# Kernel optimization log

Measured on AMD Instinct MI355X. Metric: run time of the kernel, lower is better.

## Reference

```python
import jax, jax.numpy as jnp
import numpy as np

N_NODES = 100000


def _gcn_layer(x, W, b, row, col, norm, n_nodes):
    # x: [N, Fin], W: [Fin, Fout]. GCN: A_hat @ (x W) + b with symmetric norm.
    xw = x @ W                                   # [N, Fout]
    msg = xw[row] * norm[:, None]                # [E+N, Fout] gathered messages
    agg = jax.ops.segment_sum(msg, col, num_segments=n_nodes)  # scatter-add at dst
    return agg + b


def setup_inputs() -> dict:
    key = jax.random.key(0)
    ks = jax.random.split(key, 5)
    N, E = N_NODES, 1600000
    Fin, F1, F2, C = 512, 64, 128, 40
    x = jax.random.normal(ks[0], (N, Fin), dtype=jnp.float32)
    edge_index = jax.random.randint(ks[1], (2, E), 0, N, dtype=jnp.int64)
    W1 = jax.random.normal(ks[2], (Fin, F1), dtype=jnp.float32) / np.sqrt(Fin)
    W2 = jax.random.normal(ks[3], (F1, F2), dtype=jnp.float32) / np.sqrt(F1)
    W3 = jax.random.normal(ks[4], (F2, C), dtype=jnp.float32) / np.sqrt(F2)
    return {
        "x": x, "edge_index": edge_index,
        "W1": W1, "b1": jnp.zeros((F1,), jnp.float32),
        "W2": W2, "b2": jnp.zeros((F2,), jnp.float32),
        "W3": W3, "b3": jnp.zeros((C,), jnp.float32),
    }


def reference(x, edge_index, W1, b1, W2, b2, W3, b3):
    N = x.shape[0]
    # Add self-loops (GCNConv default add_self_loops=True)
    loop = jnp.arange(N, dtype=edge_index.dtype)
    row = jnp.concatenate([edge_index[0], loop])  # source nodes
    col = jnp.concatenate([edge_index[1], loop])  # destination nodes
    # Symmetric degree normalization: deg computed at destination with self-loops
    deg = jax.ops.segment_sum(jnp.ones_like(col, dtype=x.dtype), col, num_segments=N)
    dis = jax.lax.rsqrt(deg)                      # deg >= 1 due to self-loops
    norm = dis[row] * dis[col]                    # [E+N]

    h1 = jax.nn.relu(_gcn_layer(x, W1, b1, row, col, norm, N))
    # dropout is identity (training=False)
    h2 = jax.nn.relu(_gcn_layer(h1, W2, b2, row, col, norm, N))
    h3 = _gcn_layer(h2, W3, b3, row, col, norm, N)
    return jax.nn.log_softmax(h3, axis=1)
```

## Files before the change

kernel.cpp:

```cpp
#include <hip/hip_runtime.h>
#include <math.h>


typedef __attribute__((ext_vector_type(8))) short short8;
typedef __attribute__((ext_vector_type(4))) float f32x4;

__device__ __forceinline__ unsigned short f2bf(float f) {
    unsigned int u = __float_as_uint(f);
    unsigned int r = (u + 0x7fffu + ((u >> 16) & 1u)) >> 16;
    return (unsigned short)r;
}
__device__ __forceinline__ float bflo(unsigned int u) { return __uint_as_float(u << 16); }
__device__ __forceinline__ float bfhi(unsigned int u) { return __uint_as_float(u & 0xffff0000u); }


__global__ void zero2_kernel(int* a, int* b, int n) {
    int i = blockIdx.x * 256 + threadIdx.x;
    if (i < n) { a[i] = 0; b[i] = 0; }
}

__global__ void count_kernel(const int* __restrict__ col, int* __restrict__ cnt, int E) {
    int e = blockIdx.x * 256 + threadIdx.x;
    if (e < E) atomicAdd(&cnt[col[e]], 1);
}

__global__ void scan1_kernel(const int* __restrict__ cnt, int* __restrict__ out,
                             int* __restrict__ bsums, int n) {
    __shared__ int s[1024];
    int i = blockIdx.x * 1024 + threadIdx.x;
    int v = (i < n) ? cnt[i] : 0;
    s[threadIdx.x] = v;
    __syncthreads();
    for (int off = 1; off < 1024; off <<= 1) {
        int t = 0;
        if ((int)threadIdx.x >= off) t = s[threadIdx.x - off];
        __syncthreads();
        if ((int)threadIdx.x >= off) s[threadIdx.x] += t;
        __syncthreads();
    }
    if (i < n) out[i] = s[threadIdx.x] - v;
    if (threadIdx.x == 1023) bsums[blockIdx.x] = s[1023];
}

__global__ void scan2_kernel(int* bsums, int nb) {
    __shared__ int s[128];
    int v = ((int)threadIdx.x < nb) ? bsums[threadIdx.x] : 0;
    s[threadIdx.x] = v;
    __syncthreads();
    for (int off = 1; off < 128; off <<= 1) {
        int t = 0;
        if ((int)threadIdx.x >= off) t = s[threadIdx.x - off];
        __syncthreads();
        if ((int)threadIdx.x >= off) s[threadIdx.x] += t;
        __syncthreads();
    }
    if ((int)threadIdx.x < nb) bsums[threadIdx.x] = s[threadIdx.x] - v;
}

__global__ void scan3d_kernel(int* __restrict__ ptr, const int* __restrict__ bsums,
                              const int* __restrict__ cnt, float* __restrict__ dis,
                              int n, int E) {
    int i = blockIdx.x * 1024 + threadIdx.x;
    if (i < n) {
        ptr[i] += bsums[blockIdx.x];
        dis[i] = rsqrtf((float)(cnt[i] + 1));
    }
    if (i == 0) ptr[n] = E;
}

__global__ void fill_kernel(const int* __restrict__ row, const int* __restrict__ col,
                            const int* __restrict__ ptr, int* __restrict__ fillc,
                            const float* __restrict__ dis, uint2* __restrict__ csr_en, int E) {
    int e = blockIdx.x * 256 + threadIdx.x;
    if (e < E) {
        int c = col[e];
        int r = row[e];
        int p = ptr[c] + atomicAdd(&fillc[c], 1);
        uint2 en;
        en.x = (unsigned int)r;
        en.y = __float_as_uint(dis[r] * dis[c]);
        csr_en[p] = en;
    }
}

__device__ __forceinline__ void wprep_one(const float* W, unsigned short* out,
                                          int KS, int FOUT, int t) {
    int i = t & 7;
    int l = (t >> 3) & 63;
    int g = t >> 9;
    int ks = g % KS;
    int nt = g / KS;
    int k = ks * 32 + (l >> 4) * 8 + i;
    int c = nt * 16 + (l & 15);
    out[t] = (c < FOUT) ? f2bf(W[(size_t)k * FOUT + c]) : (unsigned short)0;
}

__global__ void wprep_all_kernel(const float* __restrict__ W1, const float* __restrict__ W2,
                                 const float* __restrict__ W3,
                                 unsigned short* __restrict__ Wf1, unsigned short* __restrict__ Wf2,
                                 unsigned short* __restrict__ Wf3) {
    int t = blockIdx.x * 256 + threadIdx.x;
    if (t < 32768)       wprep_one(W1, Wf1, 16, 64, t);
    else if (t < 40960)  wprep_one(W2, Wf2, 2, 128, t - 32768);
    else if (t < 47104)  wprep_one(W3, Wf3, 4, 40, t - 40960);
}

template <int K, int FOUT, int NT>
__global__ __launch_bounds__(256) void gemm1_kernel(const float* __restrict__ Ap,
                                                    const unsigned short* __restrict__ Wf,
                                                    unsigned short* __restrict__ Y, int N) {
    constexpr int KS = K / 32;
    const int lane = threadIdx.x & 63;
    const int wid = threadIdx.x >> 6;
    const int rbase = blockIdx.x * 64 + wid * 16;
    const int rA = rbase + (lane & 15);
    const bool va = rA < N;
    const int khalf = lane >> 4;

    f32x4 acc[NT];
#pragma unroll
    for (int nt = 0; nt < NT; nt++)
#pragma unroll
        for (int j = 0; j < 4; j++) acc[nt][j] = 0.f;

    for (int ks = 0; ks < KS; ks++) {
        short8 afr;
        const float4* Arow = (const float4*)(Ap + (size_t)rA * K + ks * 32 + khalf * 8);
        float4 x0, x1;
        if (va) { x0 = Arow[0]; x1 = Arow[1]; }
        else    { x0 = make_float4(0, 0, 0, 0); x1 = x0; }
        afr[0] = (short)f2bf(x0.x); afr[1] = (short)f2bf(x0.y);
        afr[2] = (short)f2bf(x0.z); afr[3] = (short)f2bf(x0.w);
        afr[4] = (short)f2bf(x1.x); afr[5] = (short)f2bf(x1.y);
        afr[6] = (short)f2bf(x1.z); afr[7] = (short)f2bf(x1.w);
#pragma unroll
        for (int nt = 0; nt < NT; nt++) {
            short8 bfr = *(const short8*)(Wf + (((size_t)nt * KS + ks) * 64 + lane) * 8);
            acc[nt] = __builtin_amdgcn_mfma_f32_16x16x32_bf16(afr, bfr, acc[nt], 0, 0, 0);
        }
    }

    const int rD0 = rbase + (lane >> 4) * 4;
    const int colb = lane & 15;
#pragma unroll
    for (int nt = 0; nt < NT; nt++) {
        int col = nt * 16 + colb;
#pragma unroll
        for (int i = 0; i < 4; i++) {
            int rD = rD0 + i;
            if (rD < N) Y[(size_t)rD * FOUT + col] = f2bf(acc[nt][i]);
        }
    }
}

__global__ __launch_bounds__(256) void gemm23_kernel(const unsigned short* __restrict__ A,
                                                     const unsigned short* __restrict__ Wf2,
                                                     const float* __restrict__ b2,
                                                     const unsigned short* __restrict__ Wf3,
                                                     unsigned short* __restrict__ Y, int N) {
    __shared__ unsigned short hs[4][16][136];
    const int lane = threadIdx.x & 63;
    const int wid = threadIdx.x >> 6;
    const int rbase = blockIdx.x * 64 + wid * 16;
    const int rA = rbase + (lane & 15);
    const bool va = rA < N;
    const int khalf = lane >> 4;

    f32x4 acc2[8];
#pragma unroll
    for (int nt = 0; nt < 8; nt++)
#pragma unroll
        for (int j = 0; j < 4; j++) acc2[nt][j] = 0.f;

#pragma unroll
    for (int ks = 0; ks < 2; ks++) {
        short8 afr;
        if (va) afr = *(const short8*)(A + (size_t)rA * 64 + ks * 32 + khalf * 8);
        else {
#pragma unroll
            for (int j = 0; j < 8; j++) afr[j] = 0;
        }
#pragma unroll
        for (int nt = 0; nt < 8; nt++) {
            short8 bfr = *(const short8*)(Wf2 + (((size_t)nt * 2 + ks) * 64 + lane) * 8);
            acc2[nt] = __builtin_amdgcn_mfma_f32_16x16x32_bf16(afr, bfr, acc2[nt], 0, 0, 0);
        }
    }

    const int rD = (lane >> 4) * 4;
    const int colb = lane & 15;
#pragma unroll
    for (int nt = 0; nt < 8; nt++) {
        int c = nt * 16 + colb;
        float bv = b2[c];
#pragma unroll
        for (int j = 0; j < 4; j++)
            hs[wid][rD + j][c] = f2bf(fmaxf(acc2[nt][j] + bv, 0.f));
    }
    __syncthreads();

    f32x4 acc3[3];
#pragma unroll
    for (int nt = 0; nt < 3; nt++)
#pragma unroll
        for (int j = 0; j < 4; j++) acc3[nt][j] = 0.f;

    const int r = lane & 15;
#pragma unroll
    for (int ks = 0; ks < 4; ks++) {
        short8 afr = *(const short8*)&hs[wid][r][ks * 32 + khalf * 8];
#pragma unroll
        for (int nt = 0; nt < 3; nt++) {
            short8 bfr = *(const short8*)(Wf3 + (((size_t)nt * 4 + ks) * 64 + lane) * 8);
            acc3[nt] = __builtin_amdgcn_mfma_f32_16x16x32_bf16(afr, bfr, acc3[nt], 0, 0, 0);
        }
    }

#pragma unroll
    for (int nt = 0; nt < 3; nt++) {
        int col = nt * 16 + colb;
        if (col < 40) {
#pragma unroll
            for (int i = 0; i < 4; i++) {
                int rr = rbase + rD + i;
                if (rr < N) Y[(size_t)rr * 40 + col] = f2bf(acc3[nt][i]);
            }
        }
    }
}

template <bool BR>
__global__ __launch_bounds__(256) void agg64_kernel(const unsigned int* __restrict__ XW,
                                                    const float* __restrict__ bias,
                                                    const int* __restrict__ ptr,
                                                    const uint2* __restrict__ EN,
                                                    unsigned int* __restrict__ Y, int N) {
    const int lane = threadIdx.x & 63;
    const int wid = threadIdx.x >> 6;
    const int n = blockIdx.x * 4 + wid;
    if (n >= N) return;
    const int s = lane >> 3;
    const int q = lane & 7;

    const int e0 = ptr[n], e1 = ptr[n + 1];
    const float selfw = 1.0f / (float)(e1 - e0 + 1);

    float acc[8];
    if (s == 0) {
        const uint4 u = *(const uint4*)(XW + (size_t)n * 32 + q * 4);
        acc[0] = selfw * bflo(u.x); acc[1] = selfw * bfhi(u.x);
        acc[2] = selfw * bflo(u.y); acc[3] = selfw * bfhi(u.y);
        acc[4] = selfw * bflo(u.z); acc[5] = selfw * bfhi(u.z);
        acc[6] = selfw * bflo(u.w); acc[7] = selfw * bfhi(u.w);
    } else {
#pragma unroll
        for (int j = 0; j < 8; j++) acc[j] = 0.f;
    }

    for (int eb = e0; eb < e1; eb += 64) {
        int cnt = e1 - eb; if (cnt > 64) cnt = 64;
        uint2 en;
        if (lane < cnt) en = EN[eb + lane];
        else { en.x = 0; en.y = 0; }
#pragma unroll 2
        for (int k = s; k < cnt; k += 8) {
            int r = __shfl((int)en.x, k);
            float nrm = __uint_as_float((unsigned int)__shfl((int)en.y, k));
            const uint4 u = *(const uint4*)(XW + (size_t)r * 32 + q * 4);
            acc[0] += nrm * bflo(u.x); acc[1] += nrm * bfhi(u.x);
            acc[2] += nrm * bflo(u.y); acc[3] += nrm * bfhi(u.y);
            acc[4] += nrm * bflo(u.z); acc[5] += nrm * bfhi(u.z);
            acc[6] += nrm * bflo(u.w); acc[7] += nrm * bfhi(u.w);
        }
    }

#pragma unroll
    for (int off = 8; off < 64; off <<= 1)
#pragma unroll
        for (int j = 0; j < 8; j++) acc[j] += __shfl_xor(acc[j], off);

    if (lane < 8) {
        float v[8];
        if (BR) {
            const float4 b0 = *((const float4*)bias + lane * 2);
            const float4 b1 = *((const float4*)bias + lane * 2 + 1);
            v[0] = fmaxf(acc[0] + b0.x, 0.f); v[1] = fmaxf(acc[1] + b0.y, 0.f);
            v[2] = fmaxf(acc[2] + b0.z, 0.f); v[3] = fmaxf(acc[3] + b0.w, 0.f);
            v[4] = fmaxf(acc[4] + b1.x, 0.f); v[5] = fmaxf(acc[5] + b1.y, 0.f);
            v[6] = fmaxf(acc[6] + b1.z, 0.f); v[7] = fmaxf(acc[7] + b1.w, 0.f);
        } else {
#pragma unroll
            for (int j = 0; j < 8; j++) v[j] = acc[j];
        }
        uint4 o;
        o.x = (unsigned int)f2bf(v[0]) | ((unsigned int)f2bf(v[1]) << 16);
        o.y = (unsigned int)f2bf(v[2]) | ((unsigned int)f2bf(v[3]) << 16);
        o.z = (unsigned int)f2bf(v[4]) | ((unsigned int)f2bf(v[5]) << 16);
        o.w = (unsigned int)f2bf(v[6]) | ((unsigned int)f2bf(v[7]) << 16);
        *(uint4*)(Y + (size_t)n * 32 + lane * 4) = o;
    }
}

__global__ __launch_bounds__(256) void agg40lsm_kernel(const unsigned int* __restrict__ XW,
                                                       const float* __restrict__ bias,
                                                       const int* __restrict__ ptr,
                                                       const uint2* __restrict__ EN,
                                                       float* __restrict__ out, int N) {
    const int lane = threadIdx.x & 63;
    const int wid = threadIdx.x >> 6;
    const int n = blockIdx.x * 4 + wid;
    if (n >= N) return;
    const int s = lane >> 4;
    const int c = lane & 15;
    const bool act = (c < 10);

    const int e0 = ptr[n], e1 = ptr[n + 1];
    const float selfw = 1.0f / (float)(e1 - e0 + 1);

    float acc[4] = {0.f, 0.f, 0.f, 0.f};
    if (s == 0 && act) {
        const uint2 u = *(const uint2*)(XW + (size_t)n * 20 + c * 2);
        acc[0] = selfw * bflo(u.x); acc[1] = selfw * bfhi(u.x);
        acc[2] = selfw * bflo(u.y); acc[3] = selfw * bfhi(u.y);
    }

    for (int eb = e0; eb < e1; eb += 64) {
        int cnt = e1 - eb; if (cnt > 64) cnt = 64;
        uint2 en;
        if (lane < cnt) en = EN[eb + lane];
        else { en.x = 0; en.y = 0; }
#pragma unroll 2
        for (int k = s; k < cnt; k += 4) {
            int r = __shfl((int)en.x, k);
            float nrm = __uint_as_float((unsigned int)__shfl((int)en.y, k));
            if (act) {
                const uint2 u = *(const uint2*)(XW + (size_t)r * 20 + c * 2);
                acc[0] += nrm * bflo(u.x); acc[1] += nrm * bfhi(u.x);
                acc[2] += nrm * bflo(u.y); acc[3] += nrm * bfhi(u.y);
            }
        }
    }

#pragma unroll
    for (int off = 16; off < 64; off <<= 1)
#pragma unroll
        for (int j = 0; j < 4; j++) acc[j] += __shfl_xor(acc[j], off);

    float v[4];
    float m = -INFINITY;
    if (lane < 16 && act) {
        const float4 b = *((const float4*)bias + c);
        v[0] = acc[0] + b.x; v[1] = acc[1] + b.y;
        v[2] = acc[2] + b.z; v[3] = acc[3] + b.w;
        m = fmaxf(fmaxf(v[0], v[1]), fmaxf(v[2], v[3]));
    }
#pragma unroll
    for (int off = 32; off; off >>= 1) m = fmaxf(m, __shfl_xor(m, off));
    float ex = 0.f;
    if (lane < 16 && act)
        ex = expf(v[0] - m) + expf(v[1] - m) + expf(v[2] - m) + expf(v[3] - m);
#pragma unroll
    for (int off = 32; off; off >>= 1) ex += __shfl_xor(ex, off);
    float ls = logf(ex);
    if (lane < 16 && act) {
        float4 o;
        o.x = v[0] - m - ls; o.y = v[1] - m - ls;
        o.z = v[2] - m - ls; o.w = v[3] - m - ls;
        *(float4*)(out + (size_t)n * 40 + c * 4) = o;
    }
}


extern "C" void kernel_launch(void* const* d_in, const int* in_sizes, int n_in,
                              void* d_out, int out_size, void* d_ws, size_t ws_size,
                              hipStream_t stream) {
    const float* x  = (const float*)d_in[0];
    const int*   ei = (const int*)d_in[1];
    const float* W1 = (const float*)d_in[2];
    const float* b1 = (const float*)d_in[3];
    const float* W2 = (const float*)d_in[4];
    const float* b2 = (const float*)d_in[5];
    const float* W3 = (const float*)d_in[6];
    const float* b3 = (const float*)d_in[7];
    const int N = in_sizes[0] / 512;
    const int E = in_sizes[1] / 2;
    const int* row = ei;
    const int* col = ei + E;

    char* p = (char*)d_ws;
    auto alloc = [&](size_t bytes) {
        void* r = (void*)p;
        p += (bytes + 255) & ~(size_t)255;
        return r;
    };
    float* dis    = (float*)alloc((size_t)N * 4);
    int*   cnt    = (int*)alloc((size_t)N * 4);
    int*   ptr    = (int*)alloc((size_t)(N + 1) * 4);
    int*   fillc  = (int*)alloc((size_t)N * 4);
    int*   bsums  = (int*)alloc(1024);
    uint2* csr_en = (uint2*)alloc((size_t)E * 8);
    unsigned short* Wf1 = (unsigned short*)alloc(4 * 16 * 64 * 8 * 2);
    unsigned short* Wf2 = (unsigned short*)alloc(8 * 2 * 64 * 8 * 2);
    unsigned short* Wf3 = (unsigned short*)alloc(3 * 4 * 64 * 8 * 2);
    unsigned short* xw1 = (unsigned short*)alloc((size_t)N * 64 * 2);
    unsigned short* h1  = (unsigned short*)alloc((size_t)N * 64 * 2);
    unsigned short* a2  = (unsigned short*)alloc((size_t)N * 64 * 2);
    unsigned short* xw3 = (unsigned short*)alloc((size_t)N * 40 * 2);
    float* out = (float*)d_out;

    zero2_kernel<<<(N + 255) / 256, 256, 0, stream>>>(cnt, fillc, N);
    count_kernel<<<(E + 255) / 256, 256, 0, stream>>>(col, cnt, E);
    int nb = (N + 1023) / 1024;
    scan1_kernel<<<nb, 1024, 0, stream>>>(cnt, ptr, bsums, N);
    scan2_kernel<<<1, 128, 0, stream>>>(bsums, nb);
    scan3d_kernel<<<nb, 1024, 0, stream>>>(ptr, bsums, cnt, dis, N, E);
    fill_kernel<<<(E + 255) / 256, 256, 0, stream>>>(row, col, ptr, fillc, dis, csr_en, E);

    wprep_all_kernel<<<(47104 + 255) / 256, 256, 0, stream>>>(W1, W2, W3, Wf1, Wf2, Wf3);

    const int ggrid = (N + 63) / 64;
    const int ngrid = (N + 3) / 4;

    gemm1_kernel<512, 64, 4><<<ggrid, 256, 0, stream>>>(x, Wf1, xw1, N);
    agg64_kernel<true><<<ngrid, 256, 0, stream>>>((const unsigned int*)xw1, b1, ptr, csr_en,
                                                  (unsigned int*)h1, N);
    agg64_kernel<false><<<ngrid, 256, 0, stream>>>((const unsigned int*)h1, nullptr, ptr, csr_en,
                                                   (unsigned int*)a2, N);
    gemm23_kernel<<<ggrid, 256, 0, stream>>>(a2, Wf2, b2, Wf3, xw3, N);
    agg40lsm_kernel<<<ngrid, 256, 0, stream>>>((const unsigned int*)xw3, b3, ptr, csr_en, out, N);
}
```

Baseline: 379.1 us.

## Fuse degree count into GEMM1 launch and widen per-lane aggregation work

Zeroing of the count buffers moves into the weight-prep kernel. The destination-degree atomic count now runs as extra blocks inside the first GEMM launch, so the count and the GEMM can overlap and two launches go away. Both aggregation kernels change their lane mapping: 4 lanes now cover one row and 16 edges are processed in parallel per wavefront, with more features per lane. This raises memory-level parallelism on the gathers, at the cost of more registers and longer shuffle reductions.

```diff
diff --git a/kernel.cpp b/kernel.cpp
--- a/kernel.cpp
+++ b/kernel.cpp
@@ -13,15 +13,29 @@
 __device__ __forceinline__ float bflo(unsigned int u) { return __uint_as_float(u << 16); }
 __device__ __forceinline__ float bfhi(unsigned int u) { return __uint_as_float(u & 0xffff0000u); }
 
-
-__global__ void zero2_kernel(int* a, int* b, int n) {
-    int i = blockIdx.x * 256 + threadIdx.x;
-    if (i < n) { a[i] = 0; b[i] = 0; }
-}
-
-__global__ void count_kernel(const int* __restrict__ col, int* __restrict__ cnt, int E) {
-    int e = blockIdx.x * 256 + threadIdx.x;
-    if (e < E) atomicAdd(&cnt[col[e]], 1);
+__device__ __forceinline__ void wprep_one(const float* W, unsigned short* out,
+                                          int KS, int FOUT, int t) {
+    int i = t & 7;
+    int l = (t >> 3) & 63;
+    int g = t >> 9;
+    int ks = g % KS;
+    int nt = g / KS;
+    int k = ks * 32 + (l >> 4) * 8 + i;
+    int c = nt * 16 + (l & 15);
+    out[t] = (c < FOUT) ? f2bf(W[(size_t)k * FOUT + c]) : (unsigned short)0;
+}
+
+__global__ void prep_kernel(const float* __restrict__ W1, const float* __restrict__ W2,
+                            const float* __restrict__ W3,
+                            unsigned short* __restrict__ Wf1, unsigned short* __restrict__ Wf2,
+                            unsigned short* __restrict__ Wf3,
+                            int* __restrict__ cnt, int* __restrict__ fillc, int N) {
+    int t = blockIdx.x * 256 + threadIdx.x;
+    if (t < 32768)       wprep_one(W1, Wf1, 16, 64, t);
+    else if (t < 40960)  wprep_one(W2, Wf2, 2, 128, t - 32768);
+    else if (t < 47104)  wprep_one(W3, Wf3, 4, 40, t - 40960);
+    if (t < N) cnt[t] = 0;
+    else if (t < 2 * N) fillc[t - N] = 0;
 }
 
 __global__ void scan1_kernel(const int* __restrict__ cnt, int* __restrict__ out,
@@ -83,36 +97,22 @@
     }
 }
 
-__device__ __forceinline__ void wprep_one(const float* W, unsigned short* out,
-                                          int KS, int FOUT, int t) {
-    int i = t & 7;
-    int l = (t >> 3) & 63;
-    int g = t >> 9;
-    int ks = g % KS;
-    int nt = g / KS;
-    int k = ks * 32 + (l >> 4) * 8 + i;
-    int c = nt * 16 + (l & 15);
-    out[t] = (c < FOUT) ? f2bf(W[(size_t)k * FOUT + c]) : (unsigned short)0;
-}
-
-__global__ void wprep_all_kernel(const float* __restrict__ W1, const float* __restrict__ W2,
-                                 const float* __restrict__ W3,
-                                 unsigned short* __restrict__ Wf1, unsigned short* __restrict__ Wf2,
-                                 unsigned short* __restrict__ Wf3) {
-    int t = blockIdx.x * 256 + threadIdx.x;
-    if (t < 32768)       wprep_one(W1, Wf1, 16, 64, t);
-    else if (t < 40960)  wprep_one(W2, Wf2, 2, 128, t - 32768);
-    else if (t < 47104)  wprep_one(W3, Wf3, 4, 40, t - 40960);
-}
-
-template <int K, int FOUT, int NT>
-__global__ __launch_bounds__(256) void gemm1_kernel(const float* __restrict__ Ap,
-                                                    const unsigned short* __restrict__ Wf,
-                                                    unsigned short* __restrict__ Y, int N) {
-    constexpr int KS = K / 32;
+__global__ __launch_bounds__(256) void gemm1c_kernel(const float* __restrict__ Ap,
+                                                     const unsigned short* __restrict__ Wf,
+                                                     unsigned short* __restrict__ Y, int N,
+                                                     const int* __restrict__ col,
+                                                     int* __restrict__ cnt, int E, int cgrid) {
+    int bid = blockIdx.x;
+    if (bid < cgrid) {
+        int e = bid * 256 + threadIdx.x;
+        if (e < E) atomicAdd(&cnt[col[e]], 1);
+        return;
+    }
+    bid -= cgrid;
+    constexpr int K = 512, FOUT = 64, NT = 4, KS = K / 32;
     const int lane = threadIdx.x & 63;
     const int wid = threadIdx.x >> 6;
-    const int rbase = blockIdx.x * 64 + wid * 16;
+    const int rbase = bid * 64 + wid * 16;
     const int rA = rbase + (lane & 15);
     const bool va = rA < N;
     const int khalf = lane >> 4;
@@ -144,11 +144,11 @@
     const int colb = lane & 15;
 #pragma unroll
     for (int nt = 0; nt < NT; nt++) {
-        int col = nt * 16 + colb;
+        int c = nt * 16 + colb;
 #pragma unroll
         for (int i = 0; i < 4; i++) {
             int rD = rD0 + i;
-            if (rD < N) Y[(size_t)rD * FOUT + col] = f2bf(acc[nt][i]);
+            if (rD < N) Y[(size_t)rD * FOUT + c] = f2bf(acc[nt][i]);
         }
     }
 }
@@ -218,12 +218,12 @@
 
 #pragma unroll
     for (int nt = 0; nt < 3; nt++) {
-        int col = nt * 16 + colb;
-        if (col < 40) {
+        int c = nt * 16 + colb;
+        if (c < 40) {
 #pragma unroll
             for (int i = 0; i < 4; i++) {
                 int rr = rbase + rD + i;
-                if (rr < N) Y[(size_t)rr * 40 + col] = f2bf(acc3[nt][i]);
+                if (rr < N) Y[(size_t)rr * 40 + c] = f2bf(acc3[nt][i]);
             }
         }
     }
@@ -239,22 +239,27 @@
     const int wid = threadIdx.x >> 6;
     const int n = blockIdx.x * 4 + wid;
     if (n >= N) return;
-    const int s = lane >> 3;
-    const int q = lane & 7;
+    const int s = lane >> 2;
+    const int q = lane & 3;
 
     const int e0 = ptr[n], e1 = ptr[n + 1];
     const float selfw = 1.0f / (float)(e1 - e0 + 1);
 
-    float acc[8];
+    float acc[16];
     if (s == 0) {
-        const uint4 u = *(const uint4*)(XW + (size_t)n * 32 + q * 4);
-        acc[0] = selfw * bflo(u.x); acc[1] = selfw * bfhi(u.x);
-        acc[2] = selfw * bflo(u.y); acc[3] = selfw * bfhi(u.y);
-        acc[4] = selfw * bflo(u.z); acc[5] = selfw * bfhi(u.z);
-        acc[6] = selfw * bflo(u.w); acc[7] = selfw * bfhi(u.w);
+        const uint4 u0 = *(const uint4*)(XW + (size_t)n * 32 + q * 4);
+        const uint4 u1 = *(const uint4*)(XW + (size_t)n * 32 + 16 + q * 4);
+        acc[0] = selfw * bflo(u0.x); acc[1] = selfw * bfhi(u0.x);
+        acc[2] = selfw * bflo(u0.y); acc[3] = selfw * bfhi(u0.y);
+        acc[4] = selfw * bflo(u0.z); acc[5] = selfw * bfhi(u0.z);
+        acc[6] = selfw * bflo(u0.w); acc[7] = selfw * bfhi(u0.w);
+        acc[8]  = selfw * bflo(u1.x); acc[9]  = selfw * bfhi(u1.x);
+        acc[10] = selfw * bflo(u1.y); acc[11] = selfw * bfhi(u1.y);
+        acc[12] = selfw * bflo(u1.z); acc[13] = selfw * bfhi(u1.z);
+        acc[14] = selfw * bflo(u1.w); acc[15] = selfw * bfhi(u1.w);
     } else {
 #pragma unroll
-        for (int j = 0; j < 8; j++) acc[j] = 0.f;
+        for (int j = 0; j < 16; j++) acc[j] = 0.f;
     }
 
     for (int eb = e0; eb < e1; eb += 64) {
@@ -263,41 +268,57 @@
         if (lane < cnt) en = EN[eb + lane];
         else { en.x = 0; en.y = 0; }
 #pragma unroll 2
-        for (int k = s; k < cnt; k += 8) {
+        for (int k = s; k < cnt; k += 16) {
             int r = __shfl((int)en.x, k);
             float nrm = __uint_as_float((unsigned int)__shfl((int)en.y, k));
-            const uint4 u = *(const uint4*)(XW + (size_t)r * 32 + q * 4);
-            acc[0] += nrm * bflo(u.x); acc[1] += nrm * bfhi(u.x);
-            acc[2] += nrm * bflo(u.y); acc[3] += nrm * bfhi(u.y);
-            acc[4] += nrm * bflo(u.z); acc[5] += nrm * bfhi(u.z);
-            acc[6] += nrm * bflo(u.w); acc[7] += nrm * bfhi(u.w);
-        }
-    }
-
-#pragma unroll
-    for (int off = 8; off < 64; off <<= 1)
-#pragma unroll
-        for (int j = 0; j < 8; j++) acc[j] += __shfl_xor(acc[j], off);
-
-    if (lane < 8) {
-        float v[8];
+            const uint4 u0 = *(const uint4*)(XW + (size_t)r * 32 + q * 4);
+            const uint4 u1 = *(const uint4*)(XW + (size_t)r * 32 + 16 + q * 4);
+            acc[0] += nrm * bflo(u0.x); acc[1] += nrm * bfhi(u0.x);
+            acc[2] += nrm * bflo(u0.y); acc[3] += nrm * bfhi(u0.y);
+            acc[4] += nrm * bflo(u0.z); acc[5] += nrm * bfhi(u0.z);
+            acc[6] += nrm * bflo(u0.w); acc[7] += nrm * bfhi(u0.w);
+            acc[8]  += nrm * bflo(u1.x); acc[9]  += nrm * bfhi(u1.x);
+            acc[10] += nrm * bflo(u1.y); acc[11] += nrm * bfhi(u1.y);
+            acc[12] += nrm * bflo(u1.z); acc[13] += nrm * bfhi(u1.z);
+            acc[14] += nrm * bflo(u1.w); acc[15] += nrm * bfhi(u1.w);
+        }
+    }
+
+#pragma unroll
+    for (int off = 4; off < 64; off <<= 1)
+#pragma unroll
+        for (int j = 0; j < 16; j++) acc[j] += __shfl_xor(acc[j], off);
+
+    if (lane < 4) {
+        float v[16];
         if (BR) {
-            const float4 b0 = *((const float4*)bias + lane * 2);
-            const float4 b1 = *((const float4*)bias + lane * 2 + 1);
-            v[0] = fmaxf(acc[0] + b0.x, 0.f); v[1] = fmaxf(acc[1] + b0.y, 0.f);
-            v[2] = fmaxf(acc[2] + b0.z, 0.f); v[3] = fmaxf(acc[3] + b0.w, 0.f);
-            v[4] = fmaxf(acc[4] + b1.x, 0.f); v[5] = fmaxf(acc[5] + b1.y, 0.f);
-            v[6] = fmaxf(acc[6] + b1.z, 0.f); v[7] = fmaxf(acc[7] + b1.w, 0.f);
+            const float4 b0 = ((const float4*)bias)[2 * q];
+            const float4 b1 = ((const float4*)bias)[2 * q + 1];
+            const float4 b2 = ((const float4*)bias)[8 + 2 * q];
+            const float4 b3 = ((const float4*)bias)[9 + 2 * q];
+            v[0] = fmaxf(acc[0] + b0.x, 0.f);  v[1] = fmaxf(acc[1] + b0.y, 0.f);
+            v[2] = fmaxf(acc[2] + b0.z, 0.f);  v[3] = fmaxf(acc[3] + b0.w, 0.f);
+            v[4] = fmaxf(acc[4] + b1.x, 0.f);  v[5] = fmaxf(acc[5] + b1.y, 0.f);
+            v[6] = fmaxf(acc[6] + b1.z, 0.f);  v[7] = fmaxf(acc[7] + b1.w, 0.f);
+            v[8]  = fmaxf(acc[8] + b2.x, 0.f); v[9]  = fmaxf(acc[9] + b2.y, 0.f);
+            v[10] = fmaxf(acc[10] + b2.z, 0.f); v[11] = fmaxf(acc[11] + b2.w, 0.f);
+            v[12] = fmaxf(acc[12] + b3.x, 0.f); v[13] = fmaxf(acc[13] + b3.y, 0.f);
+            v[14] = fmaxf(acc[14] + b3.z, 0.f); v[15] = fmaxf(acc[15] + b3.w, 0.f);
         } else {
 #pragma unroll
-            for (int j = 0; j < 8; j++) v[j] = acc[j];
-        }
-        uint4 o;
-        o.x = (unsigned int)f2bf(v[0]) | ((unsigned int)f2bf(v[1]) << 16);
-        o.y = (unsigned int)f2bf(v[2]) | ((unsigned int)f2bf(v[3]) << 16);
-        o.z = (unsigned int)f2bf(v[4]) | ((unsigned int)f2bf(v[5]) << 16);
-        o.w = (unsigned int)f2bf(v[6]) | ((unsigned int)f2bf(v[7]) << 16);
-        *(uint4*)(Y + (size_t)n * 32 + lane * 4) = o;
+            for (int j = 0; j < 16; j++) v[j] = acc[j];
+        }
+        uint4 o0, o1;
+        o0.x = (unsigned int)f2bf(v[0]) | ((unsigned int)f2bf(v[1]) << 16);
+        o0.y = (unsigned int)f2bf(v[2]) | ((unsigned int)f2bf(v[3]) << 16);
+        o0.z = (unsigned int)f2bf(v[4]) | ((unsigned int)f2bf(v[5]) << 16);
+        o0.w = (unsigned int)f2bf(v[6]) | ((unsigned int)f2bf(v[7]) << 16);
+        o1.x = (unsigned int)f2bf(v[8])  | ((unsigned int)f2bf(v[9]) << 16);
+        o1.y = (unsigned int)f2bf(v[10]) | ((unsigned int)f2bf(v[11]) << 16);
+        o1.z = (unsigned int)f2bf(v[12]) | ((unsigned int)f2bf(v[13]) << 16);
+        o1.w = (unsigned int)f2bf(v[14]) | ((unsigned int)f2bf(v[15]) << 16);
+        *(uint4*)(Y + (size_t)n * 32 + q * 4) = o0;
+        *(uint4*)(Y + (size_t)n * 32 + 16 + q * 4) = o1;
     }
 }
 
@@ -310,18 +331,24 @@
     const int wid = threadIdx.x >> 6;
     const int n = blockIdx.x * 4 + wid;
     if (n >= N) return;
-    const int s = lane >> 4;
-    const int c = lane & 15;
-    const bool act = (c < 10);
+    const int s = lane >> 2;
+    const int q = lane & 3;
 
     const int e0 = ptr[n], e1 = ptr[n + 1];
     const float selfw = 1.0f / (float)(e1 - e0 + 1);
 
-    float acc[4] = {0.f, 0.f, 0.f, 0.f};
-    if (s == 0 && act) {
-        const uint2 u = *(const uint2*)(XW + (size_t)n * 20 + c * 2);
-        acc[0] = selfw * bflo(u.x); acc[1] = selfw * bfhi(u.x);
-        acc[2] = selfw * bflo(u.y); acc[3] = selfw * bfhi(u.y);
+    float acc[10];
+    if (s == 0) {
+        const uint4 u0 = *(const uint4*)(XW + (size_t)n * 20 + q * 4);
+        const unsigned int u2 = XW[(size_t)n * 20 + 16 + q];
+        acc[0] = selfw * bflo(u0.x); acc[1] = selfw * bfhi(u0.x);
+        acc[2] = selfw * bflo(u0.y); acc[3] = selfw * bfhi(u0.y);
+        acc[4] = selfw * bflo(u0.z); acc[5] = selfw * bfhi(u0.z);
+        acc[6] = selfw * bflo(u0.w); acc[7] = selfw * bfhi(u0.w);
+        acc[8] = selfw * bflo(u2);   acc[9] = selfw * bfhi(u2);
+    } else {
+#pragma unroll
+        for (int j = 0; j < 10; j++) acc[j] = 0.f;
     }
 
     for (int eb = e0; eb < e1; eb += 64) {
@@ -330,43 +357,59 @@
         if (lane < cnt) en = EN[eb + lane];
         else { en.x = 0; en.y = 0; }
 #pragma unroll 2
-        for (int k = s; k < cnt; k += 4) {
+        for (int k = s; k < cnt; k += 16) {
             int r = __shfl((int)en.x, k);
             float nrm = __uint_as_float((unsigned int)__shfl((int)en.y, k));
-            if (act) {
-                const uint2 u = *(const uint2*)(XW + (size_t)r * 20 + c * 2);
-                acc[0] += nrm * bflo(u.x); acc[1] += nrm * bfhi(u.x);
-                acc[2] += nrm * bflo(u.y); acc[3] += nrm * bfhi(u.y);
-            }
-        }
-    }
-
-#pragma unroll
-    for (int off = 16; off < 64; off <<= 1)
-#pragma unroll
-        for (int j = 0; j < 4; j++) acc[j] += __shfl_xor(acc[j], off);
-
-    float v[4];
+            const uint4 u0 = *(const uint4*)(XW + (size_t)r * 20 + q * 4);
+            const unsigned int u2 = XW[(size_t)r * 20 + 16 + q];
+            acc[0] += nrm * bflo(u0.x); acc[1] += nrm * bfhi(u0.x);
+            acc[2] += nrm * bflo(u0.y); acc[3] += nrm * bfhi(u0.y);
+            acc[4] += nrm * bflo(u0.z); acc[5] += nrm * bfhi(u0.z);
+            acc[6] += nrm * bflo(u0.w); acc[7] += nrm * bfhi(u0.w);
+            acc[8] += nrm * bflo(u2);   acc[9] += nrm * bfhi(u2);
+        }
+    }
+
+#pragma unroll
+    for (int off = 4; off < 64; off <<= 1)
+#pragma unroll
+        for (int j = 0; j < 10; j++) acc[j] += __shfl_xor(acc[j], off);
+
+    float v[10];
     float m = -INFINITY;
-    if (lane < 16 && act) {
-        const float4 b = *((const float4*)bias + c);
-        v[0] = acc[0] + b.x; v[1] = acc[1] + b.y;
-        v[2] = acc[2] + b.z; v[3] = acc[3] + b.w;
-        m = fmaxf(fmaxf(v[0], v[1]), fmaxf(v[2], v[3]));
-    }
-#pragma unroll
-    for (int off = 32; off; off >>= 1) m = fmaxf(m, __shfl_xor(m, off));
+    if (lane < 4) {
+        const float4 b0 = ((const float4*)bias)[2 * q];
+        const float4 b1 = ((const float4*)bias)[2 * q + 1];
+        const float2 b2 = ((const float2*)bias)[16 + q];
+        v[0] = acc[0] + b0.x; v[1] = acc[1] + b0.y;
+        v[2] = acc[2] + b0.z; v[3] = acc[3] + b0.w;
+        v[4] = acc[4] + b1.x; v[5] = acc[5] + b1.y;
+        v[6] = acc[6] + b1.z; v[7] = acc[7] + b1.w;
+        v[8] = acc[8] + b2.x; v[9] = acc[9] + b2.y;
+        m = v[0];
+#pragma unroll
+        for (int j = 1; j < 10; j++) m = fmaxf(m, v[j]);
+    }
+    m = fmaxf(m, __shfl_xor(m, 1));
+    m = fmaxf(m, __shfl_xor(m, 2));
     float ex = 0.f;
-    if (lane < 16 && act)
-        ex = expf(v[0] - m) + expf(v[1] - m) + expf(v[2] - m) + expf(v[3] - m);
-#pragma unroll
-    for (int off = 32; off; off >>= 1) ex += __shfl_xor(ex, off);
+    if (lane < 4) {
+#pragma unroll
+        for (int j = 0; j < 10; j++) ex += expf(v[j] - m);
+    }
+    ex += __shfl_xor(ex, 1);
+    ex += __shfl_xor(ex, 2);
     float ls = logf(ex);
-    if (lane < 16 && act) {
-        float4 o;
-        o.x = v[0] - m - ls; o.y = v[1] - m - ls;
-        o.z = v[2] - m - ls; o.w = v[3] - m - ls;
-        *(float4*)(out + (size_t)n * 40 + c * 4) = o;
+    if (lane < 4) {
+        float4 o0, o1; float2 o2;
+        o0.x = v[0] - m - ls; o0.y = v[1] - m - ls;
+        o0.z = v[2] - m - ls; o0.w = v[3] - m - ls;
+        o1.x = v[4] - m - ls; o1.y = v[5] - m - ls;
+        o1.z = v[6] - m - ls; o1.w = v[7] - m - ls;
+        o2.x = v[8] - m - ls; o2.y = v[9] - m - ls;
+        *(float4*)(out + (size_t)n * 40 + 8 * q) = o0;
+        *(float4*)(out + (size_t)n * 40 + 8 * q + 4) = o1;
+        *(float2*)(out + (size_t)n * 40 + 32 + 2 * q) = o2;
     }
 }
 
@@ -408,20 +451,21 @@
     unsigned short* xw3 = (unsigned short*)alloc((size_t)N * 40 * 2);
     float* out = (float*)d_out;
 
-    zero2_kernel<<<(N + 255) / 256, 256, 0, stream>>>(cnt, fillc, N);
-    count_kernel<<<(E + 255) / 256, 256, 0, stream>>>(col, cnt, E);
+    prep_kernel<<<(2 * N + 255) / 256, 256, 0, stream>>>(W1, W2, W3, Wf1, Wf2, Wf3,
+                                                         cnt, fillc, N);
+
+    const int cgrid = (E + 255) / 256;
+    const int ggrid = (N + 63) / 64;
+    gemm1c_kernel<<<cgrid + ggrid, 256, 0, stream>>>(x, Wf1, xw1, N, col, cnt, E, cgrid);
+
     int nb = (N + 1023) / 1024;
     scan1_kernel<<<nb, 1024, 0, stream>>>(cnt, ptr, bsums, N);
     scan2_kernel<<<1, 128, 0, stream>>>(bsums, nb);
     scan3d_kernel<<<nb, 1024, 0, stream>>>(ptr, bsums, cnt, dis, N, E);
-    fill_kernel<<<(E + 255) / 256, 256, 0, stream>>>(row, col, ptr, fillc, dis, csr_en, E);
-
-    wprep_all_kernel<<<(47104 + 255) / 256, 256, 0, stream>>>(W1, W2, W3, Wf1, Wf2, Wf3);
-
-    const int ggrid = (N + 63) / 64;
+    fill_kernel<<<cgrid, 256, 0, stream>>>(row, col, ptr, fillc, dis, csr_en, E);
+
     const int ngrid = (N + 3) / 4;
 
-    gemm1_kernel<512, 64, 4><<<ggrid, 256, 0, stream>>>(x, Wf1, xw1, N);
     agg64_kernel<true><<<ngrid, 256, 0, stream>>>((const unsigned int*)xw1, b1, ptr, csr_en,
                                                   (unsigned int*)h1, N);
     agg64_kernel<false><<<ngrid, 256, 0, stream>>>((const unsigned int*)h1, nullptr, ptr, csr_en,
```

New measurement: 433.4 us. +14.3%, slower.

## Split gemm1 K across waves with LDS reduction and merge zero-init into weight prep

Applied to the files above, without the earlier changes.

gemm1 now gives each block 16 rows and splits the 512-deep K dimension across its four waves. Each wave loads its four K-slices up front, and the partial accumulators are reduced through shared memory by wave 0. This is meant to quadruple the number of blocks and raise memory-level parallelism for streaming the 200MB fp32 input. The zeroing of the count arrays is fused into the weight-prep kernel, and gemm1 is launched earlier, before the CSR scan. The cost is an LDS reduction, a block sync, and idle waves during the store phase.

```diff
diff --git a/kernel.cpp b/kernel.cpp
--- a/kernel.cpp
+++ b/kernel.cpp
@@ -13,10 +13,29 @@
 __device__ __forceinline__ float bflo(unsigned int u) { return __uint_as_float(u << 16); }
 __device__ __forceinline__ float bfhi(unsigned int u) { return __uint_as_float(u & 0xffff0000u); }
 
-
-__global__ void zero2_kernel(int* a, int* b, int n) {
-    int i = blockIdx.x * 256 + threadIdx.x;
-    if (i < n) { a[i] = 0; b[i] = 0; }
+__device__ __forceinline__ void wprep_one(const float* W, unsigned short* out,
+                                          int KS, int FOUT, int t) {
+    int i = t & 7;
+    int l = (t >> 3) & 63;
+    int g = t >> 9;
+    int ks = g % KS;
+    int nt = g / KS;
+    int k = ks * 32 + (l >> 4) * 8 + i;
+    int c = nt * 16 + (l & 15);
+    out[t] = (c < FOUT) ? f2bf(W[(size_t)k * FOUT + c]) : (unsigned short)0;
+}
+
+__global__ void prep_kernel(const float* __restrict__ W1, const float* __restrict__ W2,
+                            const float* __restrict__ W3,
+                            unsigned short* __restrict__ Wf1, unsigned short* __restrict__ Wf2,
+                            unsigned short* __restrict__ Wf3,
+                            int* __restrict__ cnt, int* __restrict__ fillc, int N) {
+    int t = blockIdx.x * 256 + threadIdx.x;
+    if (t < 32768)       wprep_one(W1, Wf1, 16, 64, t);
+    else if (t < 40960)  wprep_one(W2, Wf2, 2, 128, t - 32768);
+    else if (t < 47104)  wprep_one(W3, Wf3, 4, 40, t - 40960);
+    if (t < N) cnt[t] = 0;
+    else if (t < 2 * N) fillc[t - N] = 0;
 }
 
 __global__ void count_kernel(const int* __restrict__ col, int* __restrict__ cnt, int E) {
@@ -83,72 +102,76 @@
     }
 }
 
-__device__ __forceinline__ void wprep_one(const float* W, unsigned short* out,
-                                          int KS, int FOUT, int t) {
-    int i = t & 7;
-    int l = (t >> 3) & 63;
-    int g = t >> 9;
-    int ks = g % KS;
-    int nt = g / KS;
-    int k = ks * 32 + (l >> 4) * 8 + i;
-    int c = nt * 16 + (l & 15);
-    out[t] = (c < FOUT) ? f2bf(W[(size_t)k * FOUT + c]) : (unsigned short)0;
-}
-
-__global__ void wprep_all_kernel(const float* __restrict__ W1, const float* __restrict__ W2,
-                                 const float* __restrict__ W3,
-                                 unsigned short* __restrict__ Wf1, unsigned short* __restrict__ Wf2,
-                                 unsigned short* __restrict__ Wf3) {
-    int t = blockIdx.x * 256 + threadIdx.x;
-    if (t < 32768)       wprep_one(W1, Wf1, 16, 64, t);
-    else if (t < 40960)  wprep_one(W2, Wf2, 2, 128, t - 32768);
-    else if (t < 47104)  wprep_one(W3, Wf3, 4, 40, t - 40960);
-}
-
-template <int K, int FOUT, int NT>
 __global__ __launch_bounds__(256) void gemm1_kernel(const float* __restrict__ Ap,
                                                     const unsigned short* __restrict__ Wf,
                                                     unsigned short* __restrict__ Y, int N) {
-    constexpr int KS = K / 32;
+    __shared__ float red[3][64][17];
     const int lane = threadIdx.x & 63;
     const int wid = threadIdx.x >> 6;
-    const int rbase = blockIdx.x * 64 + wid * 16;
+    const int rbase = blockIdx.x * 16;
     const int rA = rbase + (lane & 15);
     const bool va = rA < N;
     const int khalf = lane >> 4;
-
-    f32x4 acc[NT];
-#pragma unroll
-    for (int nt = 0; nt < NT; nt++)
+    const float* base = Ap + (size_t)rA * 512 + wid * 128 + khalf * 8;
+
+    float4 x0[4], x1[4];
+#pragma unroll
+    for (int s = 0; s < 4; s++) {
+        const float4* arow = (const float4*)(base + s * 32);
+        if (va) { x0[s] = arow[0]; x1[s] = arow[1]; }
+        else    { x0[s] = make_float4(0, 0, 0, 0); x1[s] = x0[s]; }
+    }
+
+    f32x4 acc[4];
+#pragma unroll
+    for (int nt = 0; nt < 4; nt++)
 #pragma unroll
         for (int j = 0; j < 4; j++) acc[nt][j] = 0.f;
 
-    for (int ks = 0; ks < KS; ks++) {
+#pragma unroll
+    for (int s = 0; s < 4; s++) {
         short8 afr;
-        const float4* Arow = (const float4*)(Ap + (size_t)rA * K + ks * 32 + khalf * 8);
-        float4 x0, x1;
-        if (va) { x0 = Arow[0]; x1 = Arow[1]; }
-        else    { x0 = make_float4(0, 0, 0, 0); x1 = x0; }
-        afr[0] = (short)f2bf(x0.x); afr[1] = (short)f2bf(x0.y);
-        afr[2] = (short)f2bf(x0.z); afr[3] = (short)f2bf(x0.w);
-        afr[4] = (short)f2bf(x1.x); afr[5] = (short)f2bf(x1.y);
-        afr[6] = (short)f2bf(x1.z); afr[7] = (short)f2bf(x1.w);
-#pragma unroll
-        for (int nt = 0; nt < NT; nt++) {
-            short8 bfr = *(const short8*)(Wf + (((size_t)nt * KS + ks) * 64 + lane) * 8);
+        afr[0] = (short)f2bf(x0[s].x); afr[1] = (short)f2bf(x0[s].y);
+        afr[2] = (short)f2bf(x0[s].z); afr[3] = (short)f2bf(x0[s].w);
+        afr[4] = (short)f2bf(x1[s].x); afr[5] = (short)f2bf(x1[s].y);
+        afr[6] = (short)f2bf(x1[s].z); afr[7] = (short)f2bf(x1[s].w);
+        const int ks = wid * 4 + s;
+#pragma unroll
+        for (int nt = 0; nt < 4; nt++) {
+            short8 bfr = *(const short8*)(Wf + (((size_t)nt * 16 + ks) * 64 + lane) * 8);
             acc[nt] = __builtin_amdgcn_mfma_f32_16x16x32_bf16(afr, bfr, acc[nt], 0, 0, 0);
         }
     }
 
-    const int rD0 = rbase + (lane >> 4) * 4;
-    const int colb = lane & 15;
-#pragma unroll
-    for (int nt = 0; nt < NT; nt++) {
-        int col = nt * 16 + colb;
-#pragma unroll
-        for (int i = 0; i < 4; i++) {
-            int rD = rD0 + i;
-            if (rD < N) Y[(size_t)rD * FOUT + col] = f2bf(acc[nt][i]);
+    if (wid > 0) {
+#pragma unroll
+        for (int nt = 0; nt < 4; nt++)
+#pragma unroll
+            for (int j = 0; j < 4; j++)
+                red[wid - 1][lane][nt * 4 + j] = acc[nt][j];
+    }
+    __syncthreads();
+    if (wid == 0) {
+#pragma unroll
+        for (int nt = 0; nt < 4; nt++)
+#pragma unroll
+            for (int j = 0; j < 4; j++) {
+                float v = acc[nt][j];
+                v += red[0][lane][nt * 4 + j];
+                v += red[1][lane][nt * 4 + j];
+                v += red[2][lane][nt * 4 + j];
+                acc[nt][j] = v;
+            }
+        const int rD0 = rbase + (lane >> 4) * 4;
+        const int colb = lane & 15;
+#pragma unroll
+        for (int nt = 0; nt < 4; nt++) {
+            int c = nt * 16 + colb;
+#pragma unroll
+            for (int i = 0; i < 4; i++) {
+                int rD = rD0 + i;
+                if (rD < N) Y[(size_t)rD * 64 + c] = f2bf(acc[nt][i]);
+            }
         }
     }
 }
@@ -218,12 +241,12 @@
 
 #pragma unroll
     for (int nt = 0; nt < 3; nt++) {
-        int col = nt * 16 + colb;
-        if (col < 40) {
+        int c = nt * 16 + colb;
+        if (c < 40) {
 #pragma unroll
             for (int i = 0; i < 4; i++) {
                 int rr = rbase + rD + i;
-                if (rr < N) Y[(size_t)rr * 40 + col] = f2bf(acc3[nt][i]);
+                if (rr < N) Y[(size_t)rr * 40 + c] = f2bf(acc3[nt][i]);
             }
         }
     }
@@ -408,20 +431,23 @@
     unsigned short* xw3 = (unsigned short*)alloc((size_t)N * 40 * 2);
     float* out = (float*)d_out;
 
-    zero2_kernel<<<(N + 255) / 256, 256, 0, stream>>>(cnt, fillc, N);
-    count_kernel<<<(E + 255) / 256, 256, 0, stream>>>(col, cnt, E);
+    prep_kernel<<<(2 * N + 255) / 256, 256, 0, stream>>>(W1, W2, W3, Wf1, Wf2, Wf3,
+                                                         cnt, fillc, N);
+
+    const int cgrid = (E + 255) / 256;
+    count_kernel<<<cgrid, 256, 0, stream>>>(col, cnt, E);
+
+    gemm1_kernel<<<(N + 15) / 16, 256, 0, stream>>>(x, Wf1, xw1, N);
+
     int nb = (N + 1023) / 1024;
     scan1_kernel<<<nb, 1024, 0, stream>>>(cnt, ptr, bsums, N);
     scan2_kernel<<<1, 128, 0, stream>>>(bsums, nb);
     scan3d_kernel<<<nb, 1024, 0, stream>>>(ptr, bsums, cnt, dis, N, E);
-    fill_kernel<<<(E + 255) / 256, 256, 0, stream>>>(row, col, ptr, fillc, dis, csr_en, E);
-
-    wprep_all_kernel<<<(47104 + 255) / 256, 256, 0, stream>>>(W1, W2, W3, Wf1, Wf2, Wf3);
-
+    fill_kernel<<<cgrid, 256, 0, stream>>>(row, col, ptr, fillc, dis, csr_en, E);
+
+    const int ngrid = (N + 3) / 4;
     const int ggrid = (N + 63) / 64;
-    const int ngrid = (N + 3) / 4;
-
-    gemm1_kernel<512, 64, 4><<<ggrid, 256, 0, stream>>>(x, Wf1, xw1, N);
+
     agg64_kernel<true><<<ngrid, 256, 0, stream>>>((const unsigned int*)xw1, b1, ptr, csr_en,
                                                   (unsigned int*)h1, N);
     agg64_kernel<false><<<ngrid, 256, 0, stream>>>((const unsigned int*)h1, nullptr, ptr, csr_en,
```

Result: no change. 374.6 us (-1.2%).
